# Optimization experiments

Hardware: AMD Instinct MI355X
Metric: run time of the kernel (lower is better)

The kernel has to match this reference:

```python
import jax, jax.numpy as jnp
import numpy as np

B = 262144       # batch_size
N = 64           # n_nodes in the DAG
K = 4            # max parents per node (banded DAG: parents i-K..i-1)
NH = 10          # hidden width of each CGNN_block


def setup_inputs() -> dict:
    key = jax.random.key(0)
    k_noise, k_w1, k_b1, k_w2, k_b2 = jax.random.split(key, 5)
    # DAG structure: node i's parents are max(0, i-K)..i-1, padded with -1.
    pidx = -np.ones((N, K), dtype=np.int32)
    for i in range(N):
        ps = list(range(max(0, i - K), i))
        pidx[i, :len(ps)] = ps
    noise = jax.random.normal(k_noise, (B, N), dtype=jnp.float32)
    # Per-node MLP params, padded to max input width K+1. Padded parent slots
    # feed zeros, so extra weight rows never contribute.
    W1 = jax.random.normal(k_w1, (N, K + 1, NH), dtype=jnp.float32) * 0.3
    b1 = jax.random.normal(k_b1, (N, NH), dtype=jnp.float32) * 0.1
    W2 = jax.random.normal(k_w2, (N, NH), dtype=jnp.float32) * 0.3
    b2 = jax.random.normal(k_b2, (N,), dtype=jnp.float32) * 0.1
    return {"noise": noise, "parent_idx": jnp.asarray(pidx),
            "W1": W1, "b1": b1, "W2": W2, "b2": b2}


def reference(noise, parent_idx, W1, b1, W2, b2):
    n_nodes = parent_idx.shape[0]

    def step(gen, xs):
        # gen: [B, N] generated values so far (topological order = 0..N-1)
        pidx, W1i, b1i, W2i, b2i, ncol, i = xs
        mask = (pidx >= 0).astype(gen.dtype)                # [K]
        vals = gen[:, jnp.clip(pidx, 0, None)] * mask       # [B, K]
        x = jnp.concatenate([vals, ncol[:, None]], axis=1)  # [B, K+1]
        h = jax.nn.relu(x @ W1i + b1i)                      # [B, NH]
        y = h @ W2i + b2i                                   # [B]
        return gen.at[:, i].set(y), None

    gen0 = jnp.zeros_like(noise)
    xs = (parent_idx, W1, b1, W2, b2, noise.T, jnp.arange(n_nodes))
    gen, _ = jax.lax.scan(step, gen0, xs)
    return gen  # torch.cat(self.generated, 1) -> [B, N]
```

## Files before the change

kernel.cpp:

```cpp
#include <hip/hip_runtime.h>


#define NN   64
#define KP   4
#define NHID 10

__global__ __launch_bounds__(256) void cgnn_fwd(
    const float* __restrict__ noise,
    const float* __restrict__ W1,
    const float* __restrict__ b1,
    const float* __restrict__ W2,
    const float* __restrict__ b2,
    float* __restrict__ out,
    int B)
{
    const int b = blockIdx.x * 256 + threadIdx.x;
    if (b >= B) return;

    const float4* __restrict__ noise4 =
        reinterpret_cast<const float4*>(noise) + (size_t)b * (NN / 4);
    float4* __restrict__ out4 =
        reinterpret_cast<float4*>(out) + (size_t)b * (NN / 4);

    float g[NN];

#pragma unroll
    for (int q = 0; q < NN / 4; ++q) {
        const float4 nzv = noise4[q];
        const float nz[4] = {nzv.x, nzv.y, nzv.z, nzv.w};

#pragma unroll
        for (int s = 0; s < 4; ++s) {
            const int i   = q * 4 + s;
            const int lo  = (i >= KP) ? (i - KP) : 0;
            const int len = i - lo;

            float h[NHID];
#pragma unroll
            for (int j = 0; j < NHID; ++j) h[j] = b1[i * NHID + j];

#pragma unroll
            for (int k = 0; k < KP; ++k) {
                if (k < len) {
                    const float xv = g[lo + k];
#pragma unroll
                    for (int j = 0; j < NHID; ++j)
                        h[j] = fmaf(xv, W1[(i * (KP + 1) + k) * NHID + j], h[j]);
                }
            }

            const float nv = nz[s];
#pragma unroll
            for (int j = 0; j < NHID; ++j)
                h[j] = fmaf(nv, W1[(i * (KP + 1) + KP) * NHID + j], h[j]);

            float y = b2[i];
#pragma unroll
            for (int j = 0; j < NHID; ++j)
                y = fmaf(fmaxf(h[j], 0.0f), W2[i * NHID + j], y);

            g[i] = y;
        }

        out4[q] = make_float4(g[q * 4], g[q * 4 + 1], g[q * 4 + 2], g[q * 4 + 3]);
    }
}

extern "C" void kernel_launch(void* const* d_in, const int* in_sizes, int n_in,
                              void* d_out, int out_size, void* d_ws, size_t ws_size,
                              hipStream_t stream) {
    const float* noise = (const float*)d_in[0];
    const float* W1 = (const float*)d_in[2];
    const float* b1 = (const float*)d_in[3];
    const float* W2 = (const float*)d_in[4];
    const float* b2 = (const float*)d_in[5];
    float* out = (float*)d_out;

    const int B = in_sizes[0] / NN;
    const int blocks = (B + 255) / 256;
    cgnn_fwd<<<blocks, 256, 0, stream>>>(noise, W1, b1, W2, b2, out, B);
}
```

Before: 191.2 us.

## Stage noise and output through swizzled LDS for coalesced global access

Each block loads its 256 rows of noise into shared memory with fully coalesced float4 reads, using an XOR swizzle to avoid bank conflicts. Threads then read their own row from LDS, compute, write results back to LDS, and the block stores the tile coalesced. This replaces strided per-thread row accesses to global memory. In exchange it uses 64KB of LDS per block, which can cap occupancy. It also drops the tail bounds check, assuming B is a multiple of 256.

Measured after the change: 196.3 us. 1.03x slower.

```diff
diff --git a/kernel.cpp b/kernel.cpp
--- a/kernel.cpp
+++ b/kernel.cpp
@@ -4,6 +4,7 @@
 #define NN   64
 #define KP   4
 #define NHID 10
+#define BLK  256
 
 __global__ __launch_bounds__(256) void cgnn_fwd(
     const float* __restrict__ noise,
@@ -14,19 +15,29 @@
     float* __restrict__ out,
     int B)
 {
-    const int b = blockIdx.x * 256 + threadIdx.x;
-    if (b >= B) return;
+    __shared__ float4 smem[BLK * 16];
 
-    const float4* __restrict__ noise4 =
-        reinterpret_cast<const float4*>(noise) + (size_t)b * (NN / 4);
-    float4* __restrict__ out4 =
-        reinterpret_cast<float4*>(out) + (size_t)b * (NN / 4);
+    const int tid = threadIdx.x;
+
+    const float4* __restrict__ gnoise =
+        reinterpret_cast<const float4*>(noise) + (size_t)blockIdx.x * (BLK * 16);
+    float4* __restrict__ gout =
+        reinterpret_cast<float4*>(out) + (size_t)blockIdx.x * (BLK * 16);
+
+#pragma unroll
+    for (int k = 0; k < 16; ++k) {
+        const int f = k * BLK + tid;
+        const float4 v = gnoise[f];
+        const int r = f >> 4, j = f & 15;
+        smem[r * 16 + (j ^ (r & 7))] = v;
+    }
+    __syncthreads();
 
     float g[NN];
 
 #pragma unroll
     for (int q = 0; q < NN / 4; ++q) {
-        const float4 nzv = noise4[q];
+        const float4 nzv = smem[tid * 16 + (q ^ (tid & 7))];
         const float nz[4] = {nzv.x, nzv.y, nzv.z, nzv.w};
 
 #pragma unroll
@@ -62,7 +73,16 @@
             g[i] = y;
         }
 
-        out4[q] = make_float4(g[q * 4], g[q * 4 + 1], g[q * 4 + 2], g[q * 4 + 3]);
+        smem[tid * 16 + (q ^ (tid & 7))] =
+            make_float4(g[q * 4], g[q * 4 + 1], g[q * 4 + 2], g[q * 4 + 3]);
+    }
+    __syncthreads();
+
+#pragma unroll
+    for (int k = 0; k < 16; ++k) {
+        const int f = k * BLK + tid;
+        const int r = f >> 4, j = f & 15;
+        gout[f] = smem[r * 16 + (j ^ (r & 7))];
     }
 }
 
@@ -77,6 +97,6 @@
     float* out = (float*)d_out;
 
     const int B = in_sizes[0] / NN;
-    const int blocks = (B + 255) / 256;
-    cgnn_fwd<<<blocks, 256, 0, stream>>>(noise, W1, b1, W2, b2, out, B);
+    const int blocks = B / BLK;
+    cgnn_fwd<<<blocks, BLK, 0, stream>>>(noise, W1, b1, W2, b2, out, B);
 }
```
